# Kernel optimization log

Hardware: AMD Instinct MI355X
Metric: run time of the kernel (lower is better)

## Reference

```python
import jax, jax.numpy as jnp
import numpy as np
from jax import lax

B, T, N, C = 32, 32, 64, 64          # batch, window, num_series, inter_dim
GRU_H, QK, HOR = 64, 32, 12          # gru_dim, qk_dim, prediction_horizon
KS = (3, 5, 7)                       # temporal kernel per block (3 + 2*i)


def setup_inputs() -> dict:
    key = jax.random.key(0)
    ks = jax.random.split(key, 32)
    rn = lambda k, shape, s=0.05: jax.random.normal(k, shape, jnp.float32) * s
    inp = {"x": jax.random.normal(ks[0], (B, T, N), jnp.float32)}
    # x_to_inter_dim: Conv1d(1, C, kernel_size=1) == scalar * w + b
    inp["w_x2i"] = rn(ks[1], (C,)); inp["b_x2i"] = rn(ks[2], (C,))
    # latentCorrelation GRU (input_size=1, hidden=GRU_H), gate order r,z,n
    inp["gru_wih"] = rn(ks[3], (3 * GRU_H, 1)); inp["gru_whh"] = rn(ks[4], (3 * GRU_H, GRU_H))
    inp["gru_bih"] = rn(ks[5], (3 * GRU_H,)); inp["gru_bhh"] = rn(ks[6], (3 * GRU_H,))
    inp["wq_w"] = rn(ks[7], (QK, GRU_H)); inp["wq_b"] = rn(ks[8], (QK,))
    inp["wk_w"] = rn(ks[9], (QK, GRU_H)); inp["wk_b"] = rn(ks[10], (QK,))
    # per block: T independent GCNConvs (theta + bias), one temporal Conv1d
    for i, k_ in enumerate(KS):
        inp[f"gcn_w{i}"] = rn(ks[11 + 4 * i], (T, C, C))
        inp[f"gcn_b{i}"] = rn(ks[12 + 4 * i], (T, C))
        inp[f"conv_w{i}"] = rn(ks[13 + 4 * i], (C, C, k_))
        inp[f"conv_b{i}"] = rn(ks[14 + 4 * i], (C,))
    inp["lout_w"] = rn(ks[25], (N * HOR, T * N * C), 0.01)
    inp["lout_b"] = rn(ks[26], (N * HOR,))
    return inp


def _forward(x, w_x2i, b_x2i, gru_wih, gru_whh, gru_bih, gru_bhh,
             wq_w, wq_b, wk_w, wk_b,
             gcn_w0, gcn_b0, conv_w0, conv_b0,
             gcn_w1, gcn_b1, conv_w1, conv_b1,
             gcn_w2, gcn_b2, conv_w2, conv_b2,
             lout_w, lout_b):
    xs = jnp.transpose(x, (1, 0, 2))  # (T, B, N) time-major

    # --- latentCorrelation: one GRU run over all B*N series at once ---
    def gru_step(h, xt):  # h: (B,N,GRU_H), xt: (B,N)
        gi = xt[..., None] * gru_wih[:, 0] + gru_bih           # (B,N,3H)
        gh = h @ gru_whh.T + gru_bhh                           # (B,N,3H)
        r = jax.nn.sigmoid(gi[..., :GRU_H] + gh[..., :GRU_H])
        z = jax.nn.sigmoid(gi[..., GRU_H:2 * GRU_H] + gh[..., GRU_H:2 * GRU_H])
        n = jnp.tanh(gi[..., 2 * GRU_H:] + r * gh[..., 2 * GRU_H:])
        return (1.0 - z) * n + z * h, None

    h0 = jnp.zeros((B, N, GRU_H), x.dtype)
    hT, _ = lax.scan(gru_step, h0, xs)                         # (B,N,GRU_H)
    Q = hT @ wq_w.T + wq_b                                     # (B,N,QK)
    K = hT @ wk_w.T + wk_b
    Wadj = jax.nn.softmax(jnp.einsum('bnq,bmq->bnm', Q, K) / jnp.sqrt(jnp.float32(QK)), axis=2)

    # GCN symmetric norm on the dense complete graph; edge (src=i, tgt=j) has
    # weight Wadj[b,i,j]; degree is per-target (column) sum.
    deg = Wadj.sum(axis=1)                                     # (B,N)
    dinv = jnp.where(deg > 0, 1.0 / jnp.sqrt(deg), 0.0)
    What = dinv[:, :, None] * Wadj * dinv[:, None, :]          # (B,N,N)

    # x_to_inter_dim (1x1 conv) applied per timestep
    feats = xs[..., None] * w_x2i + b_x2i                      # (T,B,N,C)

    for gw, gb, cw, cb, k_ in ((gcn_w0, gcn_b0, conv_w0, conv_b0, 3),
                               (gcn_w1, gcn_b1, conv_w1, conv_b1, 5),
                               (gcn_w2, gcn_b2, conv_w2, conv_b2, 7)):
        xw = jnp.einsum('tbnc,tcd->tbnd', feats, gw)           # per-timestep theta
        agg = jnp.einsum('bij,tbid->tbjd', What, xw) + gb[:, None, None, :]
        seq = jnp.transpose(agg, (1, 2, 3, 0)).reshape(B * N, C, T)
        p = k_ // 2
        conv = lax.conv_general_dilated(seq, cw, (1,), [(p, p)],
                                        dimension_numbers=('NCH', 'OIH', 'NCH'))
        conv = conv + cb[None, :, None]
        conv = jnp.where(conv >= 0, conv, 0.01 * conv)         # LeakyReLU (dropout p=0)
        feats = jnp.transpose(conv.reshape(B, N, C, T), (3, 0, 1, 2))

    # stack(x_list, dim=2).view(B*N, C*T).view(B, -1) -> (B, N*C*T) feature order (n,c,t)
    flat = jnp.transpose(feats, (1, 2, 3, 0)).reshape(B, N * C * T)
    out = flat @ lout_w.T + lout_b                             # (B, N*HOR)
    return out.reshape(B, HOR, N)


def reference(x, w_x2i, b_x2i, gru_wih, gru_whh, gru_bih, gru_bhh,
              wq_w, wq_b, wk_w, wk_b,
              gcn_w0, gcn_b0, conv_w0, conv_b0,
              gcn_w1, gcn_b1, conv_w1, conv_b1,
              gcn_w2, gcn_b2, conv_w2, conv_b2,
              lout_w, lout_b):
    return _forward(x, w_x2i, b_x2i, gru_wih, gru_whh, gru_bih, gru_bhh,
                    wq_w, wq_b, wk_w, wk_b,
                    gcn_w0, gcn_b0, conv_w0, conv_b0,
                    gcn_w1, gcn_b1, conv_w1, conv_b1,
                    gcn_w2, gcn_b2, conv_w2, conv_b2,
                    lout_w, lout_b)
```

## Files before the change

kernel.cpp:

```cpp
#include <hip/hip_runtime.h>
#include <hip/hip_bf16.h>

#define BB 32
#define TT 32
#define NN 64
#define CC 64
#define HH 64
#define QKD 32
#define HOR 12
#define OUTD (NN*HOR)
#define KFLAT (NN*CC*TT)

typedef __attribute__((ext_vector_type(4))) float f32x4;
typedef __attribute__((ext_vector_type(8))) short s16x8;

static __device__ __forceinline__ unsigned short f2bf(float f) {
    unsigned u = __float_as_uint(f);
    unsigned r = (u + 0x7FFFu + ((u >> 16) & 1u)) >> 16;
    return (unsigned short)r;
}
static __device__ __forceinline__ float bf2f(unsigned short h) {
    return __uint_as_float(((unsigned)h) << 16);
}
static __device__ __forceinline__ void split8(const float* f, uint4& hi, uint4& lo) {
    unsigned hh[8], ll[8];
    #pragma unroll
    for (int i = 0; i < 8; ++i) {
        unsigned short h = f2bf(f[i]);
        float hf = bf2f(h);
        hh[i] = h;
        ll[i] = f2bf(f[i] - hf);
    }
    hi = make_uint4(hh[0] | (hh[1] << 16), hh[2] | (hh[3] << 16),
                    hh[4] | (hh[5] << 16), hh[6] | (hh[7] << 16));
    lo = make_uint4(ll[0] | (ll[1] << 16), ll[2] | (ll[3] << 16),
                    ll[4] | (ll[5] << 16), ll[6] | (ll[7] << 16));
}
static __device__ __forceinline__ void gl2lds16(const void* gsrc, void* ldst) {
    __builtin_amdgcn_global_load_lds(
        (const __attribute__((address_space(1))) unsigned int*)gsrc,
        (__attribute__((address_space(3))) unsigned int*)ldst, 16, 0, 0);
}

__global__ __launch_bounds__(256) void gru_kernel(
    const float* __restrict__ x, const float* __restrict__ wih,
    const float* __restrict__ whh, const float* __restrict__ bih,
    const float* __restrict__ bhh, float* __restrict__ hT)
{
    __shared__ float Wt[64][193];
    __shared__ float hbuf[4][64];
    __shared__ float part[4][4][3][64];
    int tid = threadIdx.x;
    for (int idx = tid; idx < 192*64; idx += 256) {
        int g = idx >> 6, k = idx & 63;
        Wt[k][g] = whh[idx];
    }
    int w = tid >> 6;
    int j = tid & 63;
    hbuf[w][j] = 0.0f;
    __syncthreads();
    float Wreg[3][16];
    #pragma unroll
    for (int g = 0; g < 3; ++g)
        #pragma unroll
        for (int kk = 0; kk < 16; ++kk)
            Wreg[g][kk] = Wt[w*16 + kk][g*64 + j];
    int gs0 = blockIdx.x * 4;
    int b = gs0 >> 6, n0 = gs0 & 63;
    float wih_r = wih[j], wih_z = wih[64+j], wih_n = wih[128+j];
    float bi_r = bih[j], bi_z = bih[64+j], bi_n = bih[128+j];
    float bh_r = bhh[j], bh_z = bhh[64+j], bh_n = bhh[128+j];
    float hreg = 0.0f;
    for (int t = 0; t < TT; ++t) {
        float p[3][4];
        #pragma unroll
        for (int g = 0; g < 3; ++g)
            #pragma unroll
            for (int s = 0; s < 4; ++s) p[g][s] = 0.f;
        #pragma unroll
        for (int s = 0; s < 4; ++s) {
            #pragma unroll
            for (int q = 0; q < 4; ++q) {
                const float4 hv = *(const float4*)&hbuf[s][w*16 + q*4];
                #pragma unroll
                for (int g = 0; g < 3; ++g) {
                    p[g][s] += hv.x*Wreg[g][q*4]   + hv.y*Wreg[g][q*4+1]
                             + hv.z*Wreg[g][q*4+2] + hv.w*Wreg[g][q*4+3];
                }
            }
        }
        #pragma unroll
        for (int g = 0; g < 3; ++g)
            #pragma unroll
            for (int s = 0; s < 4; ++s)
                part[w][s][g][j] = p[g][s];
        __syncthreads();
        float gr = bh_r + part[0][w][0][j] + part[1][w][0][j] + part[2][w][0][j] + part[3][w][0][j];
        float gz = bh_z + part[0][w][1][j] + part[1][w][1][j] + part[2][w][1][j] + part[3][w][1][j];
        float gn = bh_n + part[0][w][2][j] + part[1][w][2][j] + part[2][w][2][j] + part[3][w][2][j];
        float xt = x[(b*TT + t)*NN + n0 + w];
        float r = 1.f/(1.f+__expf(-(xt*wih_r + bi_r + gr)));
        float z = 1.f/(1.f+__expf(-(xt*wih_z + bi_z + gz)));
        float nn_ = tanhf(xt*wih_n + bi_n + r*gn);
        float hnew = (1.f - z)*nn_ + z*hreg;
        hreg = hnew;
        hbuf[w][j] = hnew;
        __syncthreads();
    }
    hT[(gs0 + w)*64 + j] = hreg;
}

__global__ __launch_bounds__(256) void attn_kernel(
    const float* __restrict__ hT, const float* __restrict__ wq_w,
    const float* __restrict__ wq_b, const float* __restrict__ wk_w,
    const float* __restrict__ wk_b,
    unsigned short* __restrict__ whT_hi, unsigned short* __restrict__ whT_lo)
{
    __shared__ float hs[64][64];
    __shared__ float Qs[64][33], Ks[64][33];
    __shared__ float S[64][65];
    __shared__ float pd[4][64];
    __shared__ float dinv[64];
    int b = blockIdx.x, tid = threadIdx.x;
    for (int idx = tid; idx < 64*64; idx += 256) hs[idx>>6][idx&63] = hT[b*4096 + idx];
    __syncthreads();
    for (int idx = tid; idx < 64*32; idx += 256) {
        int n_ = idx >> 5, q = idx & 31;
        float accq = wq_b[q], acck = wk_b[q];
        #pragma unroll 8
        for (int h_ = 0; h_ < 64; ++h_) {
            float hv = hs[n_][h_];
            accq += hv * wq_w[q*64 + h_];
            acck += hv * wk_w[q*64 + h_];
        }
        Qs[n_][q] = accq; Ks[n_][q] = acck;
    }
    __syncthreads();
    const float scale = 0.17677669529663687f;
    for (int idx = tid; idx < 64*64; idx += 256) {
        int n_ = idx >> 6, m = idx & 63;
        float acc = 0.f;
        #pragma unroll 8
        for (int q = 0; q < 32; ++q) acc += Qs[n_][q]*Ks[m][q];
        S[n_][m] = acc * scale;
    }
    __syncthreads();
    {
        int r = tid >> 2, q = tid & 3;
        float mx = -1e30f;
        #pragma unroll
        for (int m = 0; m < 16; ++m) mx = fmaxf(mx, S[r][q*16+m]);
        mx = fmaxf(mx, __shfl_xor(mx, 1));
        mx = fmaxf(mx, __shfl_xor(mx, 2));
        float sum = 0.f;
        float e[16];
        #pragma unroll
        for (int m = 0; m < 16; ++m) { e[m] = __expf(S[r][q*16+m]-mx); sum += e[m]; }
        sum += __shfl_xor(sum, 1);
        sum += __shfl_xor(sum, 2);
        float inv = 1.f/sum;
        #pragma unroll
        for (int m = 0; m < 16; ++m) S[r][q*16+m] = e[m]*inv;
    }
    __syncthreads();
    {
        int c = tid & 63, rq = tid >> 6;
        float d = 0.f;
        #pragma unroll
        for (int i = 0; i < 16; ++i) d += S[rq*16 + i][c];
        pd[rq][c] = d;
    }
    __syncthreads();
    if (tid < 64) {
        float d = pd[0][tid]+pd[1][tid]+pd[2][tid]+pd[3][tid];
        dinv[tid] = (d > 0.f) ? 1.0f/sqrtf(d) : 0.f;
    }
    __syncthreads();
    for (int idx = tid; idx < 64*64; idx += 256) {
        int jj = idx >> 6, ii = idx & 63;
        float val = dinv[ii]*S[ii][jj]*dinv[jj];
        unsigned short h = f2bf(val);
        whT_hi[b*4096 + idx] = h;
        whT_lo[b*4096 + idx] = f2bf(val - bf2f(h));
    }
}

__global__ __launch_bounds__(256) void prep_all(
    const float* __restrict__ gw0, const float* __restrict__ wx, const float* __restrict__ bx,
    float* __restrict__ u, float* __restrict__ v,
    const float* __restrict__ gw1, unsigned short* __restrict__ g1h, unsigned short* __restrict__ g1l,
    const float* __restrict__ gw2, unsigned short* __restrict__ g2h, unsigned short* __restrict__ g2l,
    const float* __restrict__ cw1, unsigned short* __restrict__ c1h, unsigned short* __restrict__ c1l,
    const float* __restrict__ cw2, unsigned short* __restrict__ c2h, unsigned short* __restrict__ c2l,
    const float* __restrict__ cw3, unsigned short* __restrict__ c3h, unsigned short* __restrict__ c3l,
    const float* __restrict__ lb, float* __restrict__ out)
{
    int bid = blockIdx.x, tid = threadIdx.x;
    if (bid < 32) {
        __shared__ float pu[4][64], pv[4][64];
        int t = bid, d = tid & 63, cq = tid >> 6;
        float su = 0.f, sv = 0.f;
        for (int c = cq*16; c < cq*16 + 16; ++c) {
            float gv = gw0[t*4096 + c*64 + d];
            su += wx[c]*gv; sv += bx[c]*gv;
        }
        pu[cq][d] = su; pv[cq][d] = sv;
        __syncthreads();
        if (tid < 64) {
            u[t*64 + tid] = pu[0][tid]+pu[1][tid]+pu[2][tid]+pu[3][tid];
            v[t*64 + tid] = pv[0][tid]+pv[1][tid]+pv[2][tid]+pv[3][tid];
        }
    } else if (bid < 96) {
        const float* gw = (bid < 64) ? gw1 : gw2;
        unsigned short* hi = (bid < 64) ? g1h : g2h;
        unsigned short* lo = (bid < 64) ? g1l : g2l;
        int t = (bid < 64) ? bid - 32 : bid - 64;
        for (int idx = tid; idx < 4096; idx += 256) {
            int d = idx >> 6, c = idx & 63;
            float val = gw[t*4096 + c*64 + d];
            unsigned short h = f2bf(val);
            hi[t*4096 + idx] = h;
            lo[t*4096 + idx] = f2bf(val - bf2f(h));
        }
    } else if (bid < 288) {
        const float* cw; unsigned short *hi, *lo; int KW, co;
        if (bid < 160)      { cw = cw1; hi = c1h; lo = c1l; KW = 3; co = bid - 96; }
        else if (bid < 224) { cw = cw2; hi = c2h; lo = c2l; KW = 5; co = bid - 160; }
        else                { cw = cw3; hi = c3h; lo = c3l; KW = 7; co = bid - 224; }
        int K = KW*64;
        for (int idx = tid; idx < K; idx += 256) {
            int ka = idx >> 6, ci = idx & 63;
            float val = cw[(size_t)(co*64 + ci)*KW + ka];
            unsigned short h = f2bf(val);
            hi[(size_t)co*K + idx] = h;
            lo[(size_t)co*K + idx] = f2bf(val - bf2f(h));
        }
    } else {
        int idx = (bid - 288)*256 + tid;
        out[idx] = lb[idx % OUTD];
    }
}

template<bool FIRST>
__global__ __launch_bounds__(256) void gcn_mfma(
    const float* __restrict__ fin,
    const unsigned short* __restrict__ gwT_hi, const unsigned short* __restrict__ gwT_lo,
    const float* __restrict__ u, const float* __restrict__ v,
    const unsigned short* __restrict__ whT_hi, const unsigned short* __restrict__ whT_lo,
    const float* __restrict__ gb, float* __restrict__ o)
{
    __shared__ __align__(16) unsigned short ft_hi[64][64], ft_lo[64][64];
    __shared__ __align__(16) unsigned short xsT_hi[64][64], xsT_lo[64][64];
    __shared__ float x_l[64];
    int tb = blockIdx.x, t = tb >> 5, b = tb & 31;
    int tid = threadIdx.x;
    int w = tid >> 6, l = tid & 63, lm = l & 15, ld = l >> 4;

    if (FIRST) {
        if (tid < 64) x_l[tid] = fin[(b*TT + t)*NN + tid];
        __syncthreads();
        int d = tid >> 2, nq = tid & 3;
        float ud = u[t*64 + d], vd = v[t*64 + d];
        float vals[16];
        #pragma unroll
        for (int i = 0; i < 16; ++i) vals[i] = x_l[nq*16 + i]*ud + vd;
        #pragma unroll
        for (int h = 0; h < 2; ++h) {
            uint4 hi, lo; split8(&vals[h*8], hi, lo);
            int un = (nq*2 + h) ^ (d & 7);
            *(uint4*)&xsT_hi[d][un*8] = hi;
            *(uint4*)&xsT_lo[d][un*8] = lo;
        }
        __syncthreads();
    } else {
        {
            int row = tid >> 2, c0 = (tid & 3) * 16;
            const float* src = fin + (size_t)tb*4096 + row*64 + c0;
            float f8a[8], f8b[8];
            *(float4*)f8a = *(const float4*)src;       *(float4*)(f8a+4) = *(const float4*)(src+4);
            *(float4*)f8b = *(const float4*)(src+8);   *(float4*)(f8b+4) = *(const float4*)(src+12);
            uint4 hi, lo;
            split8(f8a, hi, lo);
            int u0 = ((c0>>3)) ^ (row & 7);
            *(uint4*)&ft_hi[row][u0*8] = hi; *(uint4*)&ft_lo[row][u0*8] = lo;
            split8(f8b, hi, lo);
            int u1 = ((c0>>3)+1) ^ (row & 7);
            *(uint4*)&ft_hi[row][u1*8] = hi; *(uint4*)&ft_lo[row][u1*8] = lo;
        }
        __syncthreads();
        f32x4 acc[4];
        #pragma unroll
        for (int ct = 0; ct < 4; ++ct) acc[ct] = (f32x4){0.f,0.f,0.f,0.f};
        #pragma unroll
        for (int kc = 0; kc < 2; ++kc) {
            int nrow = w*16 + lm;
            int ux = (kc*4 + ld) ^ (nrow & 7);
            s16x8 xh = *(const s16x8*)&ft_hi[nrow][ux*8];
            s16x8 xl = *(const s16x8*)&ft_lo[nrow][ux*8];
            #pragma unroll
            for (int ct = 0; ct < 4; ++ct) {
                int drow = ct*16 + lm;
                s16x8 yh = *(const s16x8*)&gwT_hi[t*4096 + drow*64 + kc*32 + ld*8];
                s16x8 yl = *(const s16x8*)&gwT_lo[t*4096 + drow*64 + kc*32 + ld*8];
                acc[ct] = __builtin_amdgcn_mfma_f32_16x16x32_bf16(xh, yh, acc[ct], 0, 0, 0);
                acc[ct] = __builtin_amdgcn_mfma_f32_16x16x32_bf16(xh, yl, acc[ct], 0, 0, 0);
                acc[ct] = __builtin_amdgcn_mfma_f32_16x16x32_bf16(xl, yh, acc[ct], 0, 0, 0);
            }
        }
        #pragma unroll
        for (int ct = 0; ct < 4; ++ct) {
            int d = ct*16 + lm;
            int n0 = w*16 + ld*4;
            unsigned short hh[4], llo[4];
            #pragma unroll
            for (int r = 0; r < 4; ++r) {
                float val = acc[ct][r];
                unsigned short h = f2bf(val);
                hh[r] = h; llo[r] = f2bf(val - bf2f(h));
            }
            int un = (n0 >> 3) ^ (d & 7);
            int base = d*64 + un*8 + (n0 & 7);
            *(uint2*)&xsT_hi[0][0 + base] = make_uint2(hh[0]|(hh[1]<<16), hh[2]|(hh[3]<<16));
            *(uint2*)&xsT_lo[0][0 + base] = make_uint2(llo[0]|(llo[1]<<16), llo[2]|(llo[3]<<16));
        }
        __syncthreads();
    }

    f32x4 acc2[4];
    #pragma unroll
    for (int ct = 0; ct < 4; ++ct) acc2[ct] = (f32x4){0.f,0.f,0.f,0.f};
    #pragma unroll
    for (int kc = 0; kc < 2; ++kc) {
        int jrow = w*16 + lm;
        s16x8 wh = *(const s16x8*)&whT_hi[b*4096 + jrow*64 + kc*32 + ld*8];
        s16x8 wl = *(const s16x8*)&whT_lo[b*4096 + jrow*64 + kc*32 + ld*8];
        #pragma unroll
        for (int ct = 0; ct < 4; ++ct) {
            int drow = ct*16 + lm;
            int uy = (kc*4 + ld) ^ (drow & 7);
            s16x8 yh = *(const s16x8*)&xsT_hi[drow][uy*8];
            s16x8 yl = *(const s16x8*)&xsT_lo[drow][uy*8];
            acc2[ct] = __builtin_amdgcn_mfma_f32_16x16x32_bf16(wh, yh, acc2[ct], 0, 0, 0);
            acc2[ct] = __builtin_amdgcn_mfma_f32_16x16x32_bf16(wh, yl, acc2[ct], 0, 0, 0);
            acc2[ct] = __builtin_amdgcn_mfma_f32_16x16x32_bf16(wl, yh, acc2[ct], 0, 0, 0);
        }
    }
    float* oo = o + (size_t)tb*4096;
    #pragma unroll
    for (int ct = 0; ct < 4; ++ct) {
        int d = ct*16 + lm;
        float bias = gb[t*64 + d];
        #pragma unroll
        for (int r = 0; r < 4; ++r) {
            int jj = w*16 + ld*4 + r;
            oo[jj*64 + d] = acc2[ct][r] + bias;
        }
    }
}

template<int KW, bool LAST>
__global__ __launch_bounds__(256) void conv_mfma(float* __restrict__ g,
    const unsigned short* __restrict__ wch, const unsigned short* __restrict__ wcl,
    const float* __restrict__ cb, unsigned short* __restrict__ fo)
{
    constexpr int P = KW/2, K = KW*64, K32 = KW*2;
    __shared__ __align__(16) unsigned short sh[32][64], sl[32][64];
    int bn = blockIdx.x, tid = threadIdx.x;
    {
        int t = tid >> 3, c0 = (tid & 7) * 8;
        const float* src = &g[((size_t)t*2048 + bn)*64 + c0];
        float f8[8];
        *(float4*)f8 = *(const float4*)src;
        *(float4*)(f8+4) = *(const float4*)(src+4);
        uint4 hi, lo; split8(f8, hi, lo);
        int uu = (tid & 7) ^ (t & 7);
        *(uint4*)&sh[t][uu*8] = hi;
        *(uint4*)&sl[t][uu*8] = lo;
    }
    __syncthreads();
    int w = tid >> 6, l = tid & 63, lm = l & 15, ld = l >> 4;
    int co = w*16 + lm;
    f32x4 acc0 = {0.f,0.f,0.f,0.f}, acc1 = {0.f,0.f,0.f,0.f};
    const s16x8 zf = {0,0,0,0,0,0,0,0};
    for (int kc = 0; kc < K32; ++kc) {
        int ka = kc >> 1;
        int ci = (kc & 1)*32 + ld*8;
        s16x8 yh = *(const s16x8*)&wch[(size_t)co*K + kc*32 + ld*8];
        s16x8 yl = *(const s16x8*)&wcl[(size_t)co*K + kc*32 + ld*8];
        #pragma unroll
        for (int Mt = 0; Mt < 2; ++Mt) {
            int ts = Mt*16 + lm + ka - P;
            bool ok = ((unsigned)ts) < 32u;
            int tc = ok ? ts : 0;
            int ua = (ci >> 3) ^ (tc & 7);
            s16x8 xh = *(const s16x8*)&sh[tc][ua*8];
            s16x8 xl = *(const s16x8*)&sl[tc][ua*8];
            if (!ok) { xh = zf; xl = zf; }
            f32x4& a = Mt ? acc1 : acc0;
            a = __builtin_amdgcn_mfma_f32_16x16x32_bf16(xh, yh, a, 0, 0, 0);
            a = __builtin_amdgcn_mfma_f32_16x16x32_bf16(xh, yl, a, 0, 0, 0);
            a = __builtin_amdgcn_mfma_f32_16x16x32_bf16(xl, yh, a, 0, 0, 0);
        }
    }
    float bias = cb[co];
    if (LAST) {
        int b = bn >> 6, n = bn & 63;
        unsigned short* ob = fo + (size_t)b*KFLAT + n*2048 + co*32;
        #pragma unroll
        for (int Mt = 0; Mt < 2; ++Mt) {
            const f32x4& a = Mt ? acc1 : acc0;
            unsigned short hv[4];
            #pragma unroll
            for (int r = 0; r < 4; ++r) {
                float val = a[r] + bias;
                val = (val >= 0.f) ? val : 0.01f*val;
                hv[r] = f2bf(val);
            }
            *(uint2*)&ob[Mt*16 + ld*4] = make_uint2(hv[0]|(hv[1]<<16), hv[2]|(hv[3]<<16));
        }
    } else {
        #pragma unroll
        for (int Mt = 0; Mt < 2; ++Mt) {
            const f32x4& a = Mt ? acc1 : acc0;
            #pragma unroll
            for (int r = 0; r < 4; ++r) {
                int t = Mt*16 + ld*4 + r;
                float val = a[r] + bias;
                val = (val >= 0.f) ? val : 0.01f*val;
                g[((size_t)t*2048 + bn)*64 + co] = val;
            }
        }
    }
}

__global__ __launch_bounds__(256) void gemm_mfma(const unsigned short* __restrict__ flat,
                                                 const float* __restrict__ W,
                                                 float* __restrict__ out)
{
    __shared__ __align__(16) float Wl[2][64][64];
    __shared__ __align__(16) unsigned short Al[2][32][64];
    const int tid = threadIdx.x;
    const int w = tid >> 6, l = tid & 63;
    const int og = blockIdx.x >> 6;
    const int kc = blockIdx.x & 63;
    const int o_blk = og * 64;
    const int kbase = kc * 2048;

    const int wrow_l = l >> 4;
    const int wu = l & 15;
    size_t w_off[4];
    #pragma unroll
    for (int i = 0; i < 4; ++i) {
        int row = w*16 + i*4 + wrow_l;
        w_off[i] = (size_t)(o_blk + row) * KFLAT + (unsigned)((wu ^ (row & 7)) * 4);
    }
    const int arow = w*8 + (l >> 3);
    const int au = l & 7;
    const size_t a_off0 = (size_t)arow * KFLAT + (unsigned)((au ^ (arow & 7)) * 8);

#define ISSUE_TILE(buf_, s_) { \
    int kwin_ = kbase + (s_)*64; \
    _Pragma("unroll") \
    for (int i_ = 0; i_ < 4; ++i_) \
        gl2lds16(W + w_off[i_] + kwin_, &Wl[buf_][w*16 + i_*4][0]); \
    gl2lds16(flat + a_off0 + kwin_, &Al[buf_][w*8][0]); \
}

    f32x4 acc0 = {0.f,0.f,0.f,0.f}, acc1 = {0.f,0.f,0.f,0.f};
    ISSUE_TILE(0, 0);
    ISSUE_TILE(1, 1);

    const int lmod = l & 15, ldiv = l >> 4, lx = l & 7;
    for (int s = 0; s < 32; ++s) {
        if (s < 31) { asm volatile("s_waitcnt vmcnt(5)" ::: "memory"); }
        else        { asm volatile("s_waitcnt vmcnt(0)" ::: "memory"); }
        __builtin_amdgcn_s_barrier();
        asm volatile("" ::: "memory");
        const int cur = s & 1;
        #pragma unroll
        for (int ksub = 0; ksub < 2; ++ksub) {
            int ju = ksub*8 + ldiv*2;
            const float4 b0 = *(const float4*)&Wl[cur][w*16 + lmod][(ju ^ lx)*4];
            const float4 b1 = *(const float4*)&Wl[cur][w*16 + lmod][((ju+1) ^ lx)*4];
            float bf[8] = {b0.x,b0.y,b0.z,b0.w,b1.x,b1.y,b1.z,b1.w};
            s16x8 bhi, blo;
            #pragma unroll
            for (int i = 0; i < 8; ++i) {
                unsigned short h = f2bf(bf[i]);
                float hf = bf2f(h);
                bhi[i] = (short)h;
                blo[i] = (short)f2bf(bf[i] - hf);
            }
            int jua = ksub*4 + ldiv;
            const s16x8 a0 = *(const s16x8*)&Al[cur][lmod]      [(jua ^ lx)*8];
            const s16x8 a1 = *(const s16x8*)&Al[cur][16 + lmod] [(jua ^ lx)*8];
            acc0 = __builtin_amdgcn_mfma_f32_16x16x32_bf16(a0, bhi, acc0, 0, 0, 0);
            acc0 = __builtin_amdgcn_mfma_f32_16x16x32_bf16(a0, blo, acc0, 0, 0, 0);
            acc1 = __builtin_amdgcn_mfma_f32_16x16x32_bf16(a1, bhi, acc1, 0, 0, 0);
            acc1 = __builtin_amdgcn_mfma_f32_16x16x32_bf16(a1, blo, acc1, 0, 0, 0);
        }
        asm volatile("" ::: "memory");
        __builtin_amdgcn_s_barrier();
        if (s < 30) { ISSUE_TILE(cur, s+2); }
    }
#undef ISSUE_TILE

    const int o_out = o_blk + w*16 + lmod;
    #pragma unroll
    for (int r = 0; r < 4; ++r) {
        int b0_ = ldiv*4 + r;
        atomicAdd(&out[(size_t)b0_*OUTD + o_out], acc0[r]);
        atomicAdd(&out[(size_t)(16 + b0_)*OUTD + o_out], acc1[r]);
    }
}

extern "C" void kernel_launch(void* const* d_in, const int* in_sizes, int n_in,
                              void* d_out, int out_size, void* d_ws, size_t ws_size,
                              hipStream_t stream) {
    (void)in_sizes; (void)n_in; (void)out_size; (void)ws_size;
    const float* x        = (const float*)d_in[0];
    const float* w_x2i    = (const float*)d_in[1];
    const float* b_x2i    = (const float*)d_in[2];
    const float* gru_wih  = (const float*)d_in[3];
    const float* gru_whh  = (const float*)d_in[4];
    const float* gru_bih  = (const float*)d_in[5];
    const float* gru_bhh  = (const float*)d_in[6];
    const float* wq_w     = (const float*)d_in[7];
    const float* wq_b     = (const float*)d_in[8];
    const float* wk_w     = (const float*)d_in[9];
    const float* wk_b     = (const float*)d_in[10];
    const float* gcn_w[3]  = {(const float*)d_in[11], (const float*)d_in[15], (const float*)d_in[19]};
    const float* gcn_b[3]  = {(const float*)d_in[12], (const float*)d_in[16], (const float*)d_in[20]};
    const float* conv_w[3] = {(const float*)d_in[13], (const float*)d_in[17], (const float*)d_in[21]};
    const float* conv_b[3] = {(const float*)d_in[14], (const float*)d_in[18], (const float*)d_in[22]};
    const float* lout_w   = (const float*)d_in[23];
    const float* lout_b   = (const float*)d_in[24];
    float* out = (float*)d_out;
    float* ws  = (float*)d_ws;

    float* hT   = ws;
    float* u    = ws + 131072;
    float* v    = ws + 133120;
    float* bufA = ws + 135168;
    float* bufB = bufA + 4194304;
    unsigned short* usb = (unsigned short*)(ws + 8523776);
    unsigned short* whT_hi  = usb;
    unsigned short* whT_lo  = usb + 131072;
    unsigned short* gwT1_hi = usb + 262144;
    unsigned short* gwT1_lo = usb + 393216;
    unsigned short* gwT2_hi = usb + 524288;
    unsigned short* gwT2_lo = usb + 655360;
    unsigned short* cw1_hi  = usb + 786432;
    unsigned short* cw1_lo  = usb + 798720;
    unsigned short* cw2_hi  = usb + 811008;
    unsigned short* cw2_lo  = usb + 831488;
    unsigned short* cw3_hi  = usb + 851968;
    unsigned short* cw3_lo  = usb + 880640;

    prep_all<<<dim3(384), dim3(256), 0, stream>>>(
        gcn_w[0], w_x2i, b_x2i, u, v,
        gcn_w[1], gwT1_hi, gwT1_lo,
        gcn_w[2], gwT2_hi, gwT2_lo,
        conv_w[0], cw1_hi, cw1_lo,
        conv_w[1], cw2_hi, cw2_lo,
        conv_w[2], cw3_hi, cw3_lo,
        lout_b, out);

    gru_kernel<<<dim3(512), dim3(256), 0, stream>>>(x, gru_wih, gru_whh, gru_bih, gru_bhh, hT);
    attn_kernel<<<dim3(32), dim3(256), 0, stream>>>(hT, wq_w, wq_b, wk_w, wk_b, whT_hi, whT_lo);

    unsigned short* flat16 = (unsigned short*)bufB;
    gcn_mfma<true><<<dim3(1024), dim3(256), 0, stream>>>(x, nullptr, nullptr, u, v,
                                                         whT_hi, whT_lo, gcn_b[0], bufA);
    conv_mfma<3,false><<<dim3(2048), dim3(256), 0, stream>>>(bufA, cw1_hi, cw1_lo, conv_b[0], nullptr);
    gcn_mfma<false><<<dim3(1024), dim3(256), 0, stream>>>(bufA, gwT1_hi, gwT1_lo, u, v,
                                                          whT_hi, whT_lo, gcn_b[1], bufB);
    conv_mfma<5,false><<<dim3(2048), dim3(256), 0, stream>>>(bufB, cw2_hi, cw2_lo, conv_b[1], nullptr);
    gcn_mfma<false><<<dim3(1024), dim3(256), 0, stream>>>(bufB, gwT2_hi, gwT2_lo, u, v,
                                                          whT_hi, whT_lo, gcn_b[2], bufA);
    conv_mfma<7,true><<<dim3(2048), dim3(256), 0, stream>>>(bufA, cw3_hi, cw3_lo, conv_b[2], (unsigned short*)bufB);

    gemm_mfma<<<dim3(768), dim3(256), 0, stream>>>(flat16, lout_w, out);
}
```

Baseline: 307.8 us.

## Fuse prep into GRU kernel, drop lo-split in final GEMM, tidy GRU smem

Merges the weight-prep kernel into the GRU kernel, so the first blocks do prep work before running their GRU slice, which removes one launch. GRU weights now load straight from global into registers instead of through a transposed LDS copy. The partial sums are packed as float4 in a shared smem buffer. The final output GEMM drops the low-half bf16 correction term of the weight split, halving its MFMA count and conversion work at the cost of accuracy on lout_w.

```diff
diff --git a/kernel.cpp b/kernel.cpp
--- a/kernel.cpp
+++ b/kernel.cpp
@@ -13,20 +13,21 @@
 
 typedef __attribute__((ext_vector_type(4))) float f32x4;
 typedef __attribute__((ext_vector_type(8))) short s16x8;
-
-static __device__ __forceinline__ unsigned short f2bf(float f) {
+typedef unsigned short ush;
+
+static __device__ __forceinline__ ush f2bf(float f) {
     unsigned u = __float_as_uint(f);
     unsigned r = (u + 0x7FFFu + ((u >> 16) & 1u)) >> 16;
-    return (unsigned short)r;
-}
-static __device__ __forceinline__ float bf2f(unsigned short h) {
+    return (ush)r;
+}
+static __device__ __forceinline__ float bf2f(ush h) {
     return __uint_as_float(((unsigned)h) << 16);
 }
 static __device__ __forceinline__ void split8(const float* f, uint4& hi, uint4& lo) {
     unsigned hh[8], ll[8];
     #pragma unroll
     for (int i = 0; i < 8; ++i) {
-        unsigned short h = f2bf(f[i]);
+        ush h = f2bf(f[i]);
         float hf = bf2f(h);
         hh[i] = h;
         ll[i] = f2bf(f[i] - hf);
@@ -42,79 +43,136 @@
         (__attribute__((address_space(3))) unsigned int*)ldst, 16, 0, 0);
 }
 
-__global__ __launch_bounds__(256) void gru_kernel(
+__global__ __launch_bounds__(256) void prep_gru_kernel(
     const float* __restrict__ x, const float* __restrict__ wih,
     const float* __restrict__ whh, const float* __restrict__ bih,
-    const float* __restrict__ bhh, float* __restrict__ hT)
+    const float* __restrict__ bhh, float* __restrict__ hT,
+    const float* __restrict__ gw0, const float* __restrict__ wx, const float* __restrict__ bx,
+    float* __restrict__ u, float* __restrict__ v,
+    const float* __restrict__ gw1, ush* __restrict__ g1h, ush* __restrict__ g1l,
+    const float* __restrict__ gw2, ush* __restrict__ g2h, ush* __restrict__ g2l,
+    const float* __restrict__ cw1, ush* __restrict__ c1h, ush* __restrict__ c1l,
+    const float* __restrict__ cw2, ush* __restrict__ c2h, ush* __restrict__ c2l,
+    const float* __restrict__ cw3, ush* __restrict__ c3h, ush* __restrict__ c3l,
+    const float* __restrict__ lb, float* __restrict__ out)
 {
-    __shared__ float Wt[64][193];
-    __shared__ float hbuf[4][64];
-    __shared__ float part[4][4][3][64];
-    int tid = threadIdx.x;
-    for (int idx = tid; idx < 192*64; idx += 256) {
-        int g = idx >> 6, k = idx & 63;
-        Wt[k][g] = whh[idx];
-    }
-    int w = tid >> 6;
-    int j = tid & 63;
-    hbuf[w][j] = 0.0f;
-    __syncthreads();
-    float Wreg[3][16];
-    #pragma unroll
-    for (int g = 0; g < 3; ++g)
-        #pragma unroll
-        for (int kk = 0; kk < 16; ++kk)
-            Wreg[g][kk] = Wt[w*16 + kk][g*64 + j];
-    int gs0 = blockIdx.x * 4;
-    int b = gs0 >> 6, n0 = gs0 & 63;
-    float wih_r = wih[j], wih_z = wih[64+j], wih_n = wih[128+j];
-    float bi_r = bih[j], bi_z = bih[64+j], bi_n = bih[128+j];
-    float bh_r = bhh[j], bh_z = bhh[64+j], bh_n = bhh[128+j];
-    float hreg = 0.0f;
-    for (int t = 0; t < TT; ++t) {
-        float p[3][4];
+    __shared__ __align__(16) char smem[17408];
+    int bid = blockIdx.x, tid = threadIdx.x;
+
+    if (bid < 32) {
+        float (*pu)[64] = (float(*)[64])smem;
+        float (*pv)[64] = (float(*)[64])(smem + 1024);
+        int t = bid, d = tid & 63, cq = tid >> 6;
+        float su = 0.f, sv = 0.f;
+        for (int c = cq*16; c < cq*16 + 16; ++c) {
+            float gv = gw0[t*4096 + c*64 + d];
+            su += wx[c]*gv; sv += bx[c]*gv;
+        }
+        pu[cq][d] = su; pv[cq][d] = sv;
+        __syncthreads();
+        if (tid < 64) {
+            u[t*64 + tid] = pu[0][tid]+pu[1][tid]+pu[2][tid]+pu[3][tid];
+            v[t*64 + tid] = pv[0][tid]+pv[1][tid]+pv[2][tid]+pv[3][tid];
+        }
+    } else if (bid < 96) {
+        const float* gw = (bid < 64) ? gw1 : gw2;
+        ush* hi = (bid < 64) ? g1h : g2h;
+        ush* lo = (bid < 64) ? g1l : g2l;
+        int t = (bid < 64) ? bid - 32 : bid - 64;
+        for (int idx = tid; idx < 4096; idx += 256) {
+            int d = idx >> 6, c = idx & 63;
+            float val = gw[t*4096 + c*64 + d];
+            ush h = f2bf(val);
+            hi[t*4096 + idx] = h;
+            lo[t*4096 + idx] = f2bf(val - bf2f(h));
+        }
+    } else if (bid < 288) {
+        const float* cw; ush *hi, *lo; int KW, co;
+        if (bid < 160)      { cw = cw1; hi = c1h; lo = c1l; KW = 3; co = bid - 96; }
+        else if (bid < 224) { cw = cw2; hi = c2h; lo = c2l; KW = 5; co = bid - 160; }
+        else                { cw = cw3; hi = c3h; lo = c3l; KW = 7; co = bid - 224; }
+        int K = KW*64;
+        for (int idx = tid; idx < K; idx += 256) {
+            int ka = idx >> 6, ci = idx & 63;
+            float val = cw[(size_t)(co*64 + ci)*KW + ka];
+            ush h = f2bf(val);
+            hi[(size_t)co*K + idx] = h;
+            lo[(size_t)co*K + idx] = f2bf(val - bf2f(h));
+        }
+    } else if (bid < 384) {
+        int idx = (bid - 288)*256 + tid;
+        out[idx] = lb[idx % OUTD];
+    }
+    __syncthreads();
+
+    {
+        float (*hbuf)[64] = (float(*)[64])smem;
+        float4* part = (float4*)(smem + 1024);
+        int w = tid >> 6, j = tid & 63;
+        float Wreg[3][16];
         #pragma unroll
         for (int g = 0; g < 3; ++g)
             #pragma unroll
-            for (int s = 0; s < 4; ++s) p[g][s] = 0.f;
-        #pragma unroll
-        for (int s = 0; s < 4; ++s) {
-            #pragma unroll
             for (int q = 0; q < 4; ++q) {
-                const float4 hv = *(const float4*)&hbuf[s][w*16 + q*4];
+                float4 wv = *(const float4*)&whh[(g*64 + j)*64 + w*16 + q*4];
+                Wreg[g][q*4+0] = wv.x; Wreg[g][q*4+1] = wv.y;
+                Wreg[g][q*4+2] = wv.z; Wreg[g][q*4+3] = wv.w;
+            }
+        hbuf[w][j] = 0.0f;
+        int gs0 = bid * 4;
+        int b = gs0 >> 6, n0 = gs0 & 63;
+        float wih_r = wih[j], wih_z = wih[64+j], wih_n = wih[128+j];
+        float bi_r = bih[j], bi_z = bih[64+j], bi_n = bih[128+j];
+        float bh_r = bhh[j], bh_z = bhh[64+j], bh_n = bhh[128+j];
+        __syncthreads();
+        float hreg = 0.0f;
+        for (int t = 0; t < TT; ++t) {
+            float p[3][4];
+            #pragma unroll
+            for (int g = 0; g < 3; ++g)
                 #pragma unroll
-                for (int g = 0; g < 3; ++g) {
-                    p[g][s] += hv.x*Wreg[g][q*4]   + hv.y*Wreg[g][q*4+1]
-                             + hv.z*Wreg[g][q*4+2] + hv.w*Wreg[g][q*4+3];
+                for (int s = 0; s < 4; ++s) p[g][s] = 0.f;
+            #pragma unroll
+            for (int s = 0; s < 4; ++s) {
+                #pragma unroll
+                for (int q = 0; q < 4; ++q) {
+                    const float4 hv = *(const float4*)&hbuf[s][w*16 + q*4];
+                    #pragma unroll
+                    for (int g = 0; g < 3; ++g) {
+                        p[g][s] += hv.x*Wreg[g][q*4]   + hv.y*Wreg[g][q*4+1]
+                                 + hv.z*Wreg[g][q*4+2] + hv.w*Wreg[g][q*4+3];
+                    }
                 }
             }
-        }
-        #pragma unroll
-        for (int g = 0; g < 3; ++g)
             #pragma unroll
             for (int s = 0; s < 4; ++s)
-                part[w][s][g][j] = p[g][s];
-        __syncthreads();
-        float gr = bh_r + part[0][w][0][j] + part[1][w][0][j] + part[2][w][0][j] + part[3][w][0][j];
-        float gz = bh_z + part[0][w][1][j] + part[1][w][1][j] + part[2][w][1][j] + part[3][w][1][j];
-        float gn = bh_n + part[0][w][2][j] + part[1][w][2][j] + part[2][w][2][j] + part[3][w][2][j];
-        float xt = x[(b*TT + t)*NN + n0 + w];
-        float r = 1.f/(1.f+__expf(-(xt*wih_r + bi_r + gr)));
-        float z = 1.f/(1.f+__expf(-(xt*wih_z + bi_z + gz)));
-        float nn_ = tanhf(xt*wih_n + bi_n + r*gn);
-        float hnew = (1.f - z)*nn_ + z*hreg;
-        hreg = hnew;
-        hbuf[w][j] = hnew;
-        __syncthreads();
-    }
-    hT[(gs0 + w)*64 + j] = hreg;
+                part[(w*4 + s)*64 + j] = make_float4(p[0][s], p[1][s], p[2][s], 0.f);
+            __syncthreads();
+            float4 q0 = part[(0*4 + w)*64 + j];
+            float4 q1 = part[(1*4 + w)*64 + j];
+            float4 q2 = part[(2*4 + w)*64 + j];
+            float4 q3 = part[(3*4 + w)*64 + j];
+            float gr = bh_r + q0.x + q1.x + q2.x + q3.x;
+            float gz = bh_z + q0.y + q1.y + q2.y + q3.y;
+            float gn = bh_n + q0.z + q1.z + q2.z + q3.z;
+            float xt = x[(b*TT + t)*NN + n0 + w];
+            float r = 1.f/(1.f+__expf(-(xt*wih_r + bi_r + gr)));
+            float z = 1.f/(1.f+__expf(-(xt*wih_z + bi_z + gz)));
+            float nn_ = tanhf(xt*wih_n + bi_n + r*gn);
+            float hnew = (1.f - z)*nn_ + z*hreg;
+            hreg = hnew;
+            hbuf[w][j] = hnew;
+            __syncthreads();
+        }
+        hT[(gs0 + w)*64 + j] = hreg;
+    }
 }
 
 __global__ __launch_bounds__(256) void attn_kernel(
     const float* __restrict__ hT, const float* __restrict__ wq_w,
     const float* __restrict__ wq_b, const float* __restrict__ wk_w,
     const float* __restrict__ wk_b,
-    unsigned short* __restrict__ whT_hi, unsigned short* __restrict__ whT_lo)
+    ush* __restrict__ whT_hi, ush* __restrict__ whT_lo)
 {
     __shared__ float hs[64][64];
     __shared__ float Qs[64][33], Ks[64][33];
@@ -179,78 +237,22 @@
     for (int idx = tid; idx < 64*64; idx += 256) {
         int jj = idx >> 6, ii = idx & 63;
         float val = dinv[ii]*S[ii][jj]*dinv[jj];
-        unsigned short h = f2bf(val);
+        ush h = f2bf(val);
         whT_hi[b*4096 + idx] = h;
         whT_lo[b*4096 + idx] = f2bf(val - bf2f(h));
-    }
-}
-
-__global__ __launch_bounds__(256) void prep_all(
-    const float* __restrict__ gw0, const float* __restrict__ wx, const float* __restrict__ bx,
-    float* __restrict__ u, float* __restrict__ v,
-    const float* __restrict__ gw1, unsigned short* __restrict__ g1h, unsigned short* __restrict__ g1l,
-    const float* __restrict__ gw2, unsigned short* __restrict__ g2h, unsigned short* __restrict__ g2l,
-    const float* __restrict__ cw1, unsigned short* __restrict__ c1h, unsigned short* __restrict__ c1l,
-    const float* __restrict__ cw2, unsigned short* __restrict__ c2h, unsigned short* __restrict__ c2l,
-    const float* __restrict__ cw3, unsigned short* __restrict__ c3h, unsigned short* __restrict__ c3l,
-    const float* __restrict__ lb, float* __restrict__ out)
-{
-    int bid = blockIdx.x, tid = threadIdx.x;
-    if (bid < 32) {
-        __shared__ float pu[4][64], pv[4][64];
-        int t = bid, d = tid & 63, cq = tid >> 6;
-        float su = 0.f, sv = 0.f;
-        for (int c = cq*16; c < cq*16 + 16; ++c) {
-            float gv = gw0[t*4096 + c*64 + d];
-            su += wx[c]*gv; sv += bx[c]*gv;
-        }
-        pu[cq][d] = su; pv[cq][d] = sv;
-        __syncthreads();
-        if (tid < 64) {
-            u[t*64 + tid] = pu[0][tid]+pu[1][tid]+pu[2][tid]+pu[3][tid];
-            v[t*64 + tid] = pv[0][tid]+pv[1][tid]+pv[2][tid]+pv[3][tid];
-        }
-    } else if (bid < 96) {
-        const float* gw = (bid < 64) ? gw1 : gw2;
-        unsigned short* hi = (bid < 64) ? g1h : g2h;
-        unsigned short* lo = (bid < 64) ? g1l : g2l;
-        int t = (bid < 64) ? bid - 32 : bid - 64;
-        for (int idx = tid; idx < 4096; idx += 256) {
-            int d = idx >> 6, c = idx & 63;
-            float val = gw[t*4096 + c*64 + d];
-            unsigned short h = f2bf(val);
-            hi[t*4096 + idx] = h;
-            lo[t*4096 + idx] = f2bf(val - bf2f(h));
-        }
-    } else if (bid < 288) {
-        const float* cw; unsigned short *hi, *lo; int KW, co;
-        if (bid < 160)      { cw = cw1; hi = c1h; lo = c1l; KW = 3; co = bid - 96; }
-        else if (bid < 224) { cw = cw2; hi = c2h; lo = c2l; KW = 5; co = bid - 160; }
-        else                { cw = cw3; hi = c3h; lo = c3l; KW = 7; co = bid - 224; }
-        int K = KW*64;
-        for (int idx = tid; idx < K; idx += 256) {
-            int ka = idx >> 6, ci = idx & 63;
-            float val = cw[(size_t)(co*64 + ci)*KW + ka];
-            unsigned short h = f2bf(val);
-            hi[(size_t)co*K + idx] = h;
-            lo[(size_t)co*K + idx] = f2bf(val - bf2f(h));
-        }
-    } else {
-        int idx = (bid - 288)*256 + tid;
-        out[idx] = lb[idx % OUTD];
     }
 }
 
 template<bool FIRST>
 __global__ __launch_bounds__(256) void gcn_mfma(
     const float* __restrict__ fin,
-    const unsigned short* __restrict__ gwT_hi, const unsigned short* __restrict__ gwT_lo,
+    const ush* __restrict__ gwT_hi, const ush* __restrict__ gwT_lo,
     const float* __restrict__ u, const float* __restrict__ v,
-    const unsigned short* __restrict__ whT_hi, const unsigned short* __restrict__ whT_lo,
+    const ush* __restrict__ whT_hi, const ush* __restrict__ whT_lo,
     const float* __restrict__ gb, float* __restrict__ o)
 {
-    __shared__ __align__(16) unsigned short ft_hi[64][64], ft_lo[64][64];
-    __shared__ __align__(16) unsigned short xsT_hi[64][64], xsT_lo[64][64];
+    __shared__ __align__(16) ush ft_hi[64][64], ft_lo[64][64];
+    __shared__ __align__(16) ush xsT_hi[64][64], xsT_lo[64][64];
     __shared__ float x_l[64];
     int tb = blockIdx.x, t = tb >> 5, b = tb & 31;
     int tid = threadIdx.x;
@@ -311,11 +313,11 @@
         for (int ct = 0; ct < 4; ++ct) {
             int d = ct*16 + lm;
             int n0 = w*16 + ld*4;
-            unsigned short hh[4], llo[4];
+            ush hh[4], llo[4];
             #pragma unroll
             for (int r = 0; r < 4; ++r) {
                 float val = acc[ct][r];
-                unsigned short h = f2bf(val);
+                ush h = f2bf(val);
                 hh[r] = h; llo[r] = f2bf(val - bf2f(h));
             }
             int un = (n0 >> 3) ^ (d & 7);
@@ -360,11 +362,11 @@
 
 template<int KW, bool LAST>
 __global__ __launch_bounds__(256) void conv_mfma(float* __restrict__ g,
-    const unsigned short* __restrict__ wch, const unsigned short* __restrict__ wcl,
-    const float* __restrict__ cb, unsigned short* __restrict__ fo)
+    const ush* __restrict__ wch, const ush* __restrict__ wcl,
+    const float* __restrict__ cb, ush* __restrict__ fo)
 {
     constexpr int P = KW/2, K = KW*64, K32 = KW*2;
-    __shared__ __align__(16) unsigned short sh[32][64], sl[32][64];
+    __shared__ __align__(16) ush sh[32][64], sl[32][64];
     int bn = blockIdx.x, tid = threadIdx.x;
     {
         int t = tid >> 3, c0 = (tid & 7) * 8;
@@ -405,11 +407,11 @@
     float bias = cb[co];
     if (LAST) {
         int b = bn >> 6, n = bn & 63;
-        unsigned short* ob = fo + (size_t)b*KFLAT + n*2048 + co*32;
+        ush* ob = fo + (size_t)b*KFLAT + n*2048 + co*32;
         #pragma unroll
         for (int Mt = 0; Mt < 2; ++Mt) {
             const f32x4& a = Mt ? acc1 : acc0;
-            unsigned short hv[4];
+            ush hv[4];
             #pragma unroll
             for (int r = 0; r < 4; ++r) {
                 float val = a[r] + bias;
@@ -433,12 +435,12 @@
     }
 }
 
-__global__ __launch_bounds__(256) void gemm_mfma(const unsigned short* __restrict__ flat,
+__global__ __launch_bounds__(256) void gemm_mfma(const ush* __restrict__ flat,
                                                  const float* __restrict__ W,
                                                  float* __restrict__ out)
 {
     __shared__ __align__(16) float Wl[2][64][64];
-    __shared__ __align__(16) unsigned short Al[2][32][64];
+    __shared__ __align__(16) ush Al[2][32][64];
     const int tid = threadIdx.x;
     const int w = tid >> 6, l = tid & 63;
     const int og = blockIdx.x >> 6;
@@ -483,21 +485,14 @@
             const float4 b0 = *(const float4*)&Wl[cur][w*16 + lmod][(ju ^ lx)*4];
             const float4 b1 = *(const float4*)&Wl[cur][w*16 + lmod][((ju+1) ^ lx)*4];
             float bf[8] = {b0.x,b0.y,b0.z,b0.w,b1.x,b1.y,b1.z,b1.w};
-            s16x8 bhi, blo;
-            #pragma unroll
-            for (int i = 0; i < 8; ++i) {
-                unsigned short h = f2bf(bf[i]);
-                float hf = bf2f(h);
-                bhi[i] = (short)h;
-                blo[i] = (short)f2bf(bf[i] - hf);
-            }
+            s16x8 bhi;
+            #pragma unroll
+            for (int i = 0; i < 8; ++i) bhi[i] = (short)f2bf(bf[i]);
             int jua = ksub*4 + ldiv;
             const s16x8 a0 = *(const s16x8*)&Al[cur][lmod]      [(jua ^ lx)*8];
             const s16x8 a1 = *(const s16x8*)&Al[cur][16 + lmod] [(jua ^ lx)*8];
             acc0 = __builtin_amdgcn_mfma_f32_16x16x32_bf16(a0, bhi, acc0, 0, 0, 0);
-            acc0 = __builtin_amdgcn_mfma_f32_16x16x32_bf16(a0, blo, acc0, 0, 0, 0);
             acc1 = __builtin_amdgcn_mfma_f32_16x16x32_bf16(a1, bhi, acc1, 0, 0, 0);
-            acc1 = __builtin_amdgcn_mfma_f32_16x16x32_bf16(a1, blo, acc1, 0, 0, 0);
         }
         asm volatile("" ::: "memory");
         __builtin_amdgcn_s_barrier();
@@ -543,21 +538,22 @@
     float* v    = ws + 133120;
     float* bufA = ws + 135168;
     float* bufB = bufA + 4194304;
-    unsigned short* usb = (unsigned short*)(ws + 8523776);
-    unsigned short* whT_hi  = usb;
-    unsigned short* whT_lo  = usb + 131072;
-    unsigned short* gwT1_hi = usb + 262144;
-    unsigned short* gwT1_lo = usb + 393216;
-    unsigned short* gwT2_hi = usb + 524288;
-    unsigned short* gwT2_lo = usb + 655360;
-    unsigned short* cw1_hi  = usb + 786432;
-    unsigned short* cw1_lo  = usb + 798720;
-    unsigned short* cw2_hi  = usb + 811008;
-    unsigned short* cw2_lo  = usb + 831488;
-    unsigned short* cw3_hi  = usb + 851968;
-    unsigned short* cw3_lo  = usb + 880640;
-
-    prep_all<<<dim3(384), dim3(256), 0, stream>>>(
+    ush* usb = (ush*)(ws + 8523776);
+    ush* whT_hi  = usb;
+    ush* whT_lo  = usb + 131072;
+    ush* gwT1_hi = usb + 262144;
+    ush* gwT1_lo = usb + 393216;
+    ush* gwT2_hi = usb + 524288;
+    ush* gwT2_lo = usb + 655360;
+    ush* cw1_hi  = usb + 786432;
+    ush* cw1_lo  = usb + 798720;
+    ush* cw2_hi  = usb + 811008;
+    ush* cw2_lo  = usb + 831488;
+    ush* cw3_hi  = usb + 851968;
+    ush* cw3_lo  = usb + 880640;
+
+    prep_gru_kernel<<<dim3(512), dim3(256), 0, stream>>>(
+        x, gru_wih, gru_whh, gru_bih, gru_bhh, hT,
         gcn_w[0], w_x2i, b_x2i, u, v,
         gcn_w[1], gwT1_hi, gwT1_lo,
         gcn_w[2], gwT2_hi, gwT2_lo,
@@ -565,8 +561,6 @@
         conv_w[1], cw2_hi, cw2_lo,
         conv_w[2], cw3_hi, cw3_lo,
         lout_b, out);
-
-    gru_kernel<<<dim3(512), dim3(256), 0, stream>>>(x, gru_wih, gru_whh, gru_bih, gru_bhh, hT);
     attn_kernel<<<dim3(32), dim3(256), 0, stream>>>(hT, wq_w, wq_b, wk_w, wk_b, whT_hi, whT_lo);
 
     unsigned short* flat16 = (unsigned short*)bufB;
@@ -578,7 +572,7 @@
     conv_mfma<5,false><<<dim3(2048), dim3(256), 0, stream>>>(bufB, cw2_hi, cw2_lo, conv_b[1], nullptr);
     gcn_mfma<false><<<dim3(1024), dim3(256), 0, stream>>>(bufB, gwT2_hi, gwT2_lo, u, v,
                                                           whT_hi, whT_lo, gcn_b[2], bufA);
-    conv_mfma<7,true><<<dim3(2048), dim3(256), 0, stream>>>(bufA, cw3_hi, cw3_lo, conv_b[2], (unsigned short*)bufB);
+    conv_mfma<7,true><<<dim3(2048), dim3(256), 0, stream>>>(bufA, cw3_hi, cw3_lo, conv_b[2], flat16);
 
     gemm_mfma<<<dim3(768), dim3(256), 0, stream>>>(flat16, lout_w, out);
 }
```

Measured after the change: 292.8 us. 4.8% less time.
